# Optimization experiments

Hardware: AMD Instinct MI355X
Metric: run time of the kernel (lower is better)

## Reference

```python
import jax, jax.numpy as jnp
import numpy as np

CUTOFF = 10.0
NUM_GAUSSIANS = 50
LOG2 = float(np.log(2.0))
PI = float(np.pi)


def ssp(v):
    # shifted softplus: softplus(x) - log(2)
    return jax.nn.softplus(v) - LOG2


def setup_inputs() -> dict:
    key = jax.random.key(0)
    ks = jax.random.split(key, 16)
    N, E, H, F, G, L = 10000, 320000, 128, 128, NUM_GAUSSIANS, 6
    s = 0.08  # param scale to keep activations stable over 6 layers
    return {
        "x": jax.random.randint(ks[0], (N,), 0, 100),
        "edge_index": jax.random.randint(ks[1], (2, E), 0, N),
        "edge_dist": jax.random.uniform(ks[2], (E,), jnp.float32) * CUTOFF,
        "emb": jax.random.normal(ks[3], (100, H), jnp.float32) * s,
        "mlp_w1": jax.random.normal(ks[4], (L, G, F), jnp.float32) * s,
        "mlp_b1": jnp.zeros((L, F), jnp.float32),
        "mlp_w2": jax.random.normal(ks[5], (L, F, F), jnp.float32) * s,
        "mlp_b2": jnp.zeros((L, F), jnp.float32),
        "lin1_w": jax.random.normal(ks[6], (L, H, F), jnp.float32) * s,
        "lin2_w": jax.random.normal(ks[7], (L, F, H), jnp.float32) * s,
        "lin2_b": jnp.zeros((L, H), jnp.float32),
        "lin_w": jax.random.normal(ks[8], (L, H, H), jnp.float32) * s,
        "lin_b": jnp.zeros((L, H), jnp.float32),
        "out1_w": jax.random.normal(ks[9], (H, H // 2), jnp.float32) * s,
        "out1_b": jnp.zeros((H // 2,), jnp.float32),
        "out2_w": jax.random.normal(ks[10], (H // 2, H // 2), jnp.float32) * s,
        "out2_b": jnp.zeros((H // 2,), jnp.float32),
        "ro_w": jax.random.normal(ks[11], (H // 2, 12), jnp.float32) * s,
        "ro_b": jnp.zeros((12,), jnp.float32),
    }


def reference(x, edge_index, edge_dist, emb, mlp_w1, mlp_b1, mlp_w2, mlp_b2,
              lin1_w, lin2_w, lin2_b, lin_w, lin_b,
              out1_w, out1_b, out2_w, out2_b, ro_w, ro_b):
    N = x.shape[0]
    L = mlp_w1.shape[0]
    src, dst = edge_index[0], edge_index[1]

    h = emb[x]  # [N, H]

    # Gaussian smearing of distances -> [E, G]
    offset = jnp.linspace(0.0, CUTOFF, NUM_GAUSSIANS)
    coeff = -0.5 / (offset[1] - offset[0]) ** 2
    ea = jnp.exp(coeff * (edge_dist[:, None] - offset[None, :]) ** 2)

    # cosine cutoff envelope C [E]
    C = 0.5 * (jnp.cos(edge_dist * PI / CUTOFF) + 1.0)

    for l in range(L):
        # per-edge filter: MLP(gaussian) * cutoff  -> [E, F]
        W = (ssp(ea @ mlp_w1[l] + mlp_b1[l]) @ mlp_w2[l] + mlp_b2[l]) * C[:, None]
        xf = h @ lin1_w[l]                      # [N, F] (lin1, no bias)
        msg = xf[src] * W                       # gather + elementwise [E, F]
        agg = jax.ops.segment_sum(msg, dst, num_segments=N)  # scatter-add
        conv = agg @ lin2_w[l] + lin2_b[l]      # [N, H]
        h = h + (ssp(conv) @ lin_w[l] + lin_b[l])

    t = ssp(h @ out1_w + out1_b)
    t = t @ out2_w + out2_b
    h_agg = jnp.sum(t, axis=0)                  # [H//2]
    return h_agg @ ro_w + ro_b                  # [12]
```

## Files before the change

kernel.cpp:

```cpp
#include <hip/hip_runtime.h>
#include <math.h>

#define E_NUM 320000
#define N_NUM 10000
#define NB16  (N_NUM / 16)
#define TAB   2048

typedef unsigned short ushort_t;
typedef short short8_t __attribute__((ext_vector_type(8)));
typedef float f32x4    __attribute__((ext_vector_type(4)));

#define WP_O1   294912
#define WP_O2   303104
#define WP_W1T  307200
#define WP_W2T  356352
#define WP_TOT  454656

#define HB  1250
#define PB  ((WP_TOT + 255) / 256)

#define FK_SC 625
#define FK_TB 768
#define FK_EM NB16

__device__ __forceinline__ float ssp_f(float x) {
    return fmaxf(x, 0.f) + __logf(1.f + __expf(-fabsf(x))) - 0.69314718056f;
}

__device__ __forceinline__ float bf2f(ushort_t u) {
    union { unsigned int i; float f; } v;
    v.i = ((unsigned int)u) << 16;
    return v.f;
}
__device__ __forceinline__ ushort_t f2bf(float f) {
    union { float f; unsigned int i; } v;
    v.f = f;
    unsigned int u = v.i;
    unsigned int r = (u + 0x7FFFu + ((u >> 16) & 1u)) >> 16;
    return (ushort_t)r;
}

__global__ __launch_bounds__(256) void hist_pack_kernel(const int* __restrict__ ei,
                                                        int* __restrict__ counts,
                                                        const float* __restrict__ lin2_w,
                                                        const float* __restrict__ lin_w,
                                                        const float* __restrict__ lin1_w,
                                                        const float* __restrict__ o1w,
                                                        const float* __restrict__ o2w,
                                                        const float* __restrict__ mlp_w1,
                                                        const float* __restrict__ mlp_w2,
                                                        short* __restrict__ wpack) {
    if (blockIdx.x < HB) {
        int e = blockIdx.x * 256 + threadIdx.x;
        atomicAdd(&counts[ei[E_NUM + e]], 1);
        return;
    }
    int idx = (blockIdx.x - HB) * 256 + threadIdx.x;
    const int M128 = 16384;
    if (idx < 18 * M128) {
        int g = idx / M128, r = idx % M128;
        const float* src;
        if (g < 6) src = lin2_w + g * M128;
        else if (g < 12) src = lin_w + (g - 6) * M128;
        else src = lin1_w + (g - 12) * M128;
        int j = r & 7, L = (r >> 3) & 63, ks = (r >> 9) & 3, t = r >> 11;
        int n = t * 16 + (L & 15);
        int k = ks * 32 + (L >> 4) * 8 + j;
        wpack[idx] = (short)f2bf(src[k * 128 + n]);
    } else if (idx < WP_O2) {
        int r = idx - WP_O1;
        int j = r & 7, L = (r >> 3) & 63, ks = (r >> 9) & 3, t = r >> 11;
        int n = t * 16 + (L & 15);
        int k = ks * 32 + (L >> 4) * 8 + j;
        wpack[idx] = (short)f2bf(o1w[k * 64 + n]);
    } else if (idx < WP_W1T) {
        int r = idx - WP_O2;
        int j = r & 7, L = (r >> 3) & 63, ks = (r >> 9) & 1, t = r >> 10;
        int n = t * 16 + (L & 15);
        int k = ks * 32 + (L >> 4) * 8 + j;
        wpack[idx] = (short)f2bf(o2w[k * 64 + n]);
    } else if (idx < WP_W1T + 6 * 8192 && idx >= WP_W1T) {
        int r2 = idx - WP_W1T;
        int g = r2 / 8192, r = r2 % 8192;
        int j = r & 7, L = (r >> 3) & 63, ks = (r >> 9) & 1, t = r >> 10;
        int n = t * 16 + (L & 15);
        int k = ks * 32 + (L >> 4) * 8 + j;
        float v = (k < 50) ? mlp_w1[g * 6400 + k * 128 + n] : 0.f;
        wpack[idx] = (short)f2bf(v);
    } else if (idx < WP_TOT) {
        int r2 = idx - WP_W2T;
        int g = r2 / M128, r = r2 % M128;
        int j = r & 7, L = (r >> 3) & 63, ks = (r >> 9) & 3, t = r >> 11;
        int n = t * 16 + (L & 15);
        int k = ks * 32 + (L >> 4) * 8 + j;
        wpack[idx] = (short)f2bf(mlp_w2[g * M128 + k * 128 + n]);
    }
}

__global__ __launch_bounds__(1024) void scan_kernel(const int* __restrict__ counts,
                                                    int* __restrict__ offs,
                                                    int* __restrict__ cursor) {
    __shared__ int part[1024];
    const int tid = threadIdx.x;
    const int CH = 10;
    int base = tid * CH;
    int s = 0;
    #pragma unroll
    for (int i = 0; i < CH; ++i) {
        int idx = base + i;
        if (idx < N_NUM) s += counts[idx];
    }
    part[tid] = s;
    __syncthreads();
    for (int off = 1; off < 1024; off <<= 1) {
        int v = (tid >= off) ? part[tid - off] : 0;
        __syncthreads();
        part[tid] += v;
        __syncthreads();
    }
    int run = (tid > 0) ? part[tid - 1] : 0;
    #pragma unroll
    for (int i = 0; i < CH; ++i) {
        int idx = base + i;
        if (idx < N_NUM) {
            offs[idx] = run;
            cursor[idx] = run;
            run += counts[idx];
        }
    }
    if (tid == 1023) offs[N_NUM] = part[1023];
}

__global__ __launch_bounds__(512) void front_kernel(const int* __restrict__ ei,
                                                    const float* __restrict__ dist,
                                                    int* __restrict__ cursor,
                                                    int* __restrict__ meta,
                                                    const short* __restrict__ w1t,
                                                    const float* __restrict__ mlp_b1,
                                                    const short* __restrict__ w2t,
                                                    const float* __restrict__ mlp_b2,
                                                    ushort_t* __restrict__ tabB,
                                                    const int* __restrict__ x,
                                                    const float* __restrict__ emb,
                                                    const short* __restrict__ w1p0,
                                                    float* __restrict__ h,
                                                    ushort_t* __restrict__ xf) {
    __shared__ short EA[16 * 72];
    __shared__ short HD[16 * 136];
    __shared__ int s_x[16];
    const int tid = threadIdx.x;

    if (blockIdx.x < FK_SC) {
        int e = blockIdx.x * 512 + tid;
        int d = ei[E_NUM + e];
        int pos = atomicAdd(&cursor[d], 1);
        float t = dist[e] * ((float)(TAB - 1) / 10.0f);
        int i0 = (int)(t + 0.5f);
        if (i0 > TAB - 1) i0 = TAB - 1;
        meta[pos] = (i0 << 14) | ei[e];
        return;
    }

    const int wv = tid >> 6;
    const int lane = tid & 63;
    const int m = lane & 15, q = lane >> 4;

    if (blockIdx.x < FK_SC + FK_TB) {
        const int bt = blockIdx.x - FK_SC;
        const int l = bt >> 7;
        const int r0 = (bt & 127) * 16;
        const float DG = 10.0f / (float)(TAB - 1);
        const float STEP = 10.0f / 49.0f;
        const float COEFF = -0.5f / (STEP * STEP);

        for (int i = tid; i < 16 * 64; i += 512) {
            int r = i >> 6, k = i & 63;
            float v = 0.f;
            if (k < 50) {
                float d = (float)(r0 + r) * DG;
                float t = d - (float)k * STEP;
                v = __expf(COEFF * t * t);
            }
            EA[r * 72 + k] = (short)f2bf(v);
        }
        __syncthreads();

        {
            f32x4 acc = {0.f, 0.f, 0.f, 0.f};
            #pragma unroll
            for (int ks = 0; ks < 2; ++ks) {
                short8_t a = *(const short8_t*)(EA + m * 72 + ks * 32 + q * 8);
                short8_t b = *(const short8_t*)(w1t + l * 8192 + (wv * 2 + ks) * 512 + lane * 8);
                acc = __builtin_amdgcn_mfma_f32_16x16x32_bf16(a, b, acc, 0, 0, 0);
            }
            float bv = mlp_b1[l * 128 + wv * 16 + m];
            #pragma unroll
            for (int i = 0; i < 4; ++i)
                HD[(q * 4 + i) * 136 + wv * 16 + m] = (short)f2bf(ssp_f(acc[i] + bv));
        }
        __syncthreads();

        {
            f32x4 acc = {0.f, 0.f, 0.f, 0.f};
            #pragma unroll
            for (int ks = 0; ks < 4; ++ks) {
                short8_t a = *(const short8_t*)(HD + m * 136 + ks * 32 + q * 8);
                short8_t b = *(const short8_t*)(w2t + l * 16384 + (wv * 4 + ks) * 512 + lane * 8);
                acc = __builtin_amdgcn_mfma_f32_16x16x32_bf16(a, b, acc, 0, 0, 0);
            }
            int col = wv * 16 + m;
            float bv = mlp_b2[l * 128 + col];
            ushort_t* tl = tabB + (size_t)l * TAB * 128;
            #pragma unroll
            for (int i = 0; i < 4; ++i) {
                int row = r0 + q * 4 + i;
                float d = (float)row * DG;
                float C = 0.5f * (__cosf(d * 0.31415926535f) + 1.0f);
                tl[(size_t)row * 128 + col] = f2bf((acc[i] + bv) * C);
            }
        }
        return;
    }

    {
        const int n0 = (blockIdx.x - FK_SC - FK_TB) * 16;
        if (tid < 16) s_x[tid] = x[n0 + tid];
        __syncthreads();
        {
            int r = tid >> 5;
            int c4 = (tid & 31) * 4;
            float4 v = *(const float4*)(emb + (size_t)s_x[r] * 128 + c4);
            *(float4*)(h + (size_t)(n0 + r) * 128 + c4) = v;
            short4 o;
            o.x = (short)f2bf(v.x); o.y = (short)f2bf(v.y);
            o.z = (short)f2bf(v.z); o.w = (short)f2bf(v.w);
            *(short4*)(HD + r * 136 + c4) = o;
        }
        __syncthreads();
        f32x4 acc = {0.f, 0.f, 0.f, 0.f};
        #pragma unroll
        for (int ks = 0; ks < 4; ++ks) {
            short8_t a = *(const short8_t*)(HD + m * 136 + ks * 32 + q * 8);
            short8_t b = *(const short8_t*)(w1p0 + (wv * 4 + ks) * 512 + lane * 8);
            acc = __builtin_amdgcn_mfma_f32_16x16x32_bf16(a, b, acc, 0, 0, 0);
        }
        #pragma unroll
        for (int i = 0; i < 4; ++i) {
            int grow = n0 + q * 4 + i;
            xf[(size_t)grow * 128 + wv * 16 + m] = f2bf(acc[i]);
        }
    }
}

__device__ __forceinline__ void nacc8(short8_t x, short8_t t, float* o) {
    #pragma unroll
    for (int j = 0; j < 8; ++j)
        o[j] = fmaf(bf2f((ushort_t)x[j]), bf2f((ushort_t)t[j]), o[j]);
}

template <bool LAST>
__global__ __launch_bounds__(512) void layer_kernel(const int* __restrict__ offs,
                                                    const int* __restrict__ meta,
                                                    const ushort_t* __restrict__ xf,
                                                    const ushort_t* __restrict__ tabB,
                                                    const short* __restrict__ w2p,
                                                    const float* __restrict__ lin2_b,
                                                    const short* __restrict__ wlp,
                                                    const float* __restrict__ lin_b,
                                                    const short* __restrict__ w1p,
                                                    float* __restrict__ h,
                                                    ushort_t* __restrict__ xf_out,
                                                    const short* __restrict__ o1p,
                                                    const float* __restrict__ o1b,
                                                    const short* __restrict__ o2p,
                                                    const float* __restrict__ o2b,
                                                    float* __restrict__ gs) {
    __shared__ short A1[16 * 136];
    __shared__ short A2[16 * 136];
    __shared__ float P[16 * 128];
    __shared__ float red[4][64];
    const int tid = threadIdx.x;
    const int n0 = blockIdx.x * 16;
    const int wv = tid >> 6;
    const int lane = tid & 63;
    const int strm = wv >> 2;

    {
        const int qt = lane >> 4;
        const int c8 = (lane & 15) * 8;
        const int row = (wv & 3) * 4 + qt;
        const int node = n0 + row;
        int s0 = offs[node];
        int s1 = offs[node + 1];
        int mid = s0 + ((s1 - s0) >> 1);
        int e   = strm ? mid : s0;
        int end = strm ? s1  : mid;

        float accA[8] = {0.f, 0.f, 0.f, 0.f, 0.f, 0.f, 0.f, 0.f};
        float accB[8] = {0.f, 0.f, 0.f, 0.f, 0.f, 0.f, 0.f, 0.f};

        int mc[8];
        bool have = (e + 8 <= end);
        if (have) {
            #pragma unroll
            for (int u = 0; u < 8; ++u) mc[u] = meta[e + u];
        }
        while (have) {
            bool nxt = (e + 16 <= end);
            int mn[8];
            if (nxt) {
                #pragma unroll
                for (int u = 0; u < 8; ++u) mn[u] = meta[e + 8 + u];
            }
            short8_t xv[8], tv[8];
            #pragma unroll
            for (int u = 0; u < 8; ++u) {
                xv[u] = *(const short8_t*)(xf + (size_t)(mc[u] & 0x3FFF) * 128 + c8);
                tv[u] = *(const short8_t*)(tabB + (size_t)((unsigned)mc[u] >> 14) * 128 + c8);
            }
            #pragma unroll
            for (int u = 0; u < 8; ++u)
                nacc8(xv[u], tv[u], (u & 1) ? accB : accA);
            #pragma unroll
            for (int u = 0; u < 8; ++u) mc[u] = mn[u];
            e += 8;
            have = nxt;
        }
        if (e + 4 <= end) {
            int mm[4];
            #pragma unroll
            for (int u = 0; u < 4; ++u) mm[u] = meta[e + u];
            short8_t xv[4], tv[4];
            #pragma unroll
            for (int u = 0; u < 4; ++u) {
                xv[u] = *(const short8_t*)(xf + (size_t)(mm[u] & 0x3FFF) * 128 + c8);
                tv[u] = *(const short8_t*)(tabB + (size_t)((unsigned)mm[u] >> 14) * 128 + c8);
            }
            #pragma unroll
            for (int u = 0; u < 4; ++u)
                nacc8(xv[u], tv[u], (u & 1) ? accB : accA);
            e += 4;
        }
        for (; e < end; ++e) {
            int mm = meta[e];
            short8_t xv = *(const short8_t*)(xf + (size_t)(mm & 0x3FFF) * 128 + c8);
            short8_t tv = *(const short8_t*)(tabB + (size_t)((unsigned)mm >> 14) * 128 + c8);
            nacc8(xv, tv, accA);
        }

        if (!strm) {
            #pragma unroll
            for (int j = 0; j < 8; ++j)
                P[row * 128 + c8 + j] = accA[j] + accB[j];
        }
        __syncthreads();
        if (strm) {
            short8_t out;
            #pragma unroll
            for (int j = 0; j < 8; ++j)
                out[j] = (short)f2bf(accA[j] + accB[j] + P[row * 128 + c8 + j]);
            *(short8_t*)&A1[row * 136 + c8] = out;
        }
    }
    __syncthreads();

    const int m = lane & 15, q = lane >> 4;
    const int t = wv;

    {
        f32x4 acc = {0.f, 0.f, 0.f, 0.f};
        #pragma unroll
        for (int ks = 0; ks < 4; ++ks) {
            short8_t a = *(const short8_t*)(A1 + m * 136 + ks * 32 + q * 8);
            short8_t b = *(const short8_t*)(w2p + (t * 4 + ks) * 512 + lane * 8);
            acc = __builtin_amdgcn_mfma_f32_16x16x32_bf16(a, b, acc, 0, 0, 0);
        }
        float bv = lin2_b[t * 16 + m];
        #pragma unroll
        for (int i = 0; i < 4; ++i)
            A2[(q * 4 + i) * 136 + t * 16 + m] = (short)f2bf(ssp_f(acc[i] + bv));
    }
    __syncthreads();

    {
        f32x4 acc = {0.f, 0.f, 0.f, 0.f};
        #pragma unroll
        for (int ks = 0; ks < 4; ++ks) {
            short8_t a = *(const short8_t*)(A2 + m * 136 + ks * 32 + q * 8);
            short8_t b = *(const short8_t*)(wlp + (t * 4 + ks) * 512 + lane * 8);
            acc = __builtin_amdgcn_mfma_f32_16x16x32_bf16(a, b, acc, 0, 0, 0);
        }
        float bv = lin_b[t * 16 + m];
        #pragma unroll
        for (int i = 0; i < 4; ++i) {
            int r = q * 4 + i;
            int grow = n0 + r;
            float h0 = h[(size_t)grow * 128 + t * 16 + m];
            float hn = h0 + acc[i] + bv;
            if (!LAST) h[(size_t)grow * 128 + t * 16 + m] = hn;
            A1[r * 136 + t * 16 + m] = (short)f2bf(hn);
        }
    }
    __syncthreads();

    if constexpr (!LAST) {
        f32x4 acc = {0.f, 0.f, 0.f, 0.f};
        #pragma unroll
        for (int ks = 0; ks < 4; ++ks) {
            short8_t a = *(const short8_t*)(A1 + m * 136 + ks * 32 + q * 8);
            short8_t b = *(const short8_t*)(w1p + (t * 4 + ks) * 512 + lane * 8);
            acc = __builtin_amdgcn_mfma_f32_16x16x32_bf16(a, b, acc, 0, 0, 0);
        }
        #pragma unroll
        for (int i = 0; i < 4; ++i) {
            int r = q * 4 + i;
            int grow = n0 + r;
            xf_out[(size_t)grow * 128 + t * 16 + m] = f2bf(acc[i]);
        }
    } else {
        if (wv < 4) {
            f32x4 acc = {0.f, 0.f, 0.f, 0.f};
            #pragma unroll
            for (int ks = 0; ks < 4; ++ks) {
                short8_t a = *(const short8_t*)(A1 + m * 136 + ks * 32 + q * 8);
                short8_t b = *(const short8_t*)(o1p + (wv * 4 + ks) * 512 + lane * 8);
                acc = __builtin_amdgcn_mfma_f32_16x16x32_bf16(a, b, acc, 0, 0, 0);
            }
            float bv = o1b[wv * 16 + m];
            #pragma unroll
            for (int i = 0; i < 4; ++i) {
                int r = q * 4 + i;
                A2[r * 136 + wv * 16 + m] = (short)f2bf(ssp_f(acc[i] + bv));
            }
        }
        __syncthreads();
        if (wv < 4) {
            f32x4 acc = {0.f, 0.f, 0.f, 0.f};
            #pragma unroll
            for (int ks = 0; ks < 2; ++ks) {
                short8_t a = *(const short8_t*)(A2 + m * 136 + ks * 32 + q * 8);
                short8_t b = *(const short8_t*)(o2p + (wv * 2 + ks) * 512 + lane * 8);
                acc = __builtin_amdgcn_mfma_f32_16x16x32_bf16(a, b, acc, 0, 0, 0);
            }
            float bv = o2b[wv * 16 + m];
            float part = acc[0] + acc[1] + acc[2] + acc[3] + 4.0f * bv;
            red[q][wv * 16 + m] = part;
        }
        __syncthreads();
        if (tid < 64) {
            float s = red[0][tid] + red[1][tid] + red[2][tid] + red[3][tid];
            atomicAdd(&gs[tid], s);
        }
    }
}

__global__ void final_kernel(const float* __restrict__ gs,
                             const float* __restrict__ ro_w,
                             const float* __restrict__ ro_b,
                             float* __restrict__ out) {
    int i = threadIdx.x;
    if (i < 12) {
        float s = ro_b[i];
        for (int k = 0; k < 64; ++k) s = fmaf(gs[k], ro_w[k * 12 + i], s);
        out[i] = s;
    }
}

extern "C" void kernel_launch(void* const* d_in, const int* in_sizes, int n_in,
                              void* d_out, int out_size, void* d_ws, size_t ws_size,
                              hipStream_t stream) {
    const int*   x      = (const int*)d_in[0];
    const int*   ei     = (const int*)d_in[1];
    const float* dist   = (const float*)d_in[2];
    const float* emb    = (const float*)d_in[3];
    const float* mlp_w1 = (const float*)d_in[4];
    const float* mlp_b1 = (const float*)d_in[5];
    const float* mlp_w2 = (const float*)d_in[6];
    const float* mlp_b2 = (const float*)d_in[7];
    const float* lin1_w = (const float*)d_in[8];
    const float* lin2_w = (const float*)d_in[9];
    const float* lin2_b = (const float*)d_in[10];
    const float* lin_w  = (const float*)d_in[11];
    const float* lin_b  = (const float*)d_in[12];
    const float* out1_w = (const float*)d_in[13];
    const float* out1_b = (const float*)d_in[14];
    const float* out2_w = (const float*)d_in[15];
    const float* out2_b = (const float*)d_in[16];
    const float* ro_w   = (const float*)d_in[17];
    const float* ro_b   = (const float*)d_in[18];
    float* out = (float*)d_out;

    char* base = (char*)d_ws;
    float*    h     = (float*)base;     base += (size_t)N_NUM * 128 * 4;
    ushort_t* tabB  = (ushort_t*)base;  base += (size_t)6 * TAB * 128 * 2;
    ushort_t* xf0   = (ushort_t*)base;  base += (size_t)N_NUM * 128 * 2;
    ushort_t* xf1   = (ushort_t*)base;  base += (size_t)N_NUM * 128 * 2;
    int*      meta  = (int*)base;       base += (size_t)E_NUM * 4;
    short*    wpack = (short*)base;     base += (size_t)WP_TOT * 2;
    float*    gs    = (float*)base;     base += 64 * 4;
    int*      offs  = (int*)base;       base += (N_NUM + 1) * 4;
    int*      cursor= (int*)base;       base += N_NUM * 4;
    int*      counts= (int*)base;       base += N_NUM * 4;

    hipMemsetAsync(counts, 0, N_NUM * sizeof(int), stream);
    hipMemsetAsync(gs, 0, 64 * sizeof(float), stream);

    hist_pack_kernel<<<HB + PB, 256, 0, stream>>>(
        ei, counts, lin2_w, lin_w, lin1_w, out1_w, out2_w, mlp_w1, mlp_w2, wpack);

    scan_kernel<<<1, 1024, 0, stream>>>(counts, offs, cursor);

    front_kernel<<<FK_SC + FK_TB + FK_EM, 512, 0, stream>>>(
        ei, dist, cursor, meta,
        wpack + WP_W1T, mlp_b1, wpack + WP_W2T, mlp_b2, tabB,
        x, emb, wpack + 12 * 16384, h, xf0);

    const short* o1p = wpack + WP_O1;
    const short* o2p = wpack + WP_O2;

    for (int l = 0; l < 6; ++l) {
        ushort_t* xin  = (l & 1) ? xf1 : xf0;
        ushort_t* xout = (l & 1) ? xf0 : xf1;
        const ushort_t* tl = tabB + (size_t)l * TAB * 128;
        const short* w2p = wpack + l * 16384;
        const short* wlp = wpack + (6 + l) * 16384;
        if (l < 5) {
            const short* w1p = wpack + (12 + l + 1) * 16384;
            layer_kernel<false><<<NB16, 512, 0, stream>>>(
                offs, meta, xin, tl,
                w2p, lin2_b + l * 128, wlp, lin_b + l * 128, w1p,
                h, xout, nullptr, nullptr, nullptr, nullptr, nullptr);
        } else {
            layer_kernel<true><<<NB16, 512, 0, stream>>>(
                offs, meta, xin, tl,
                w2p, lin2_b + l * 128, wlp, lin_b + l * 128, nullptr,
                h, nullptr, o1p, out1_b, o2p, out2_b, gs);
        }
    }

    final_kernel<<<1, 64, 0, stream>>>(gs, ro_w, ro_b, out);
}
```

Baseline: 288.3 us.

## Software-pipeline edge gather loop with 4-wide double buffering and occupancy hint

Restructures the per-node edge aggregation loop into a 4-edge software pipeline. The gathers for the next batch are issued before accumulating the current batch, and edge metadata is prefetched two batches ahead. The scalar tail loop becomes a single predicated 4-wide block, and launch_bounds adds a minimum of 4 blocks per CU to cap register use. The aim is to hide gather latency while keeping registers low, at the risk of spills or less memory-level parallelism than the old 8-wide batches.

```diff
diff --git a/kernel.cpp b/kernel.cpp
--- a/kernel.cpp
+++ b/kernel.cpp
@@ -259,7 +259,7 @@
 }
 
 template <bool LAST>
-__global__ __launch_bounds__(512) void layer_kernel(const int* __restrict__ offs,
+__global__ __launch_bounds__(512, 4) void layer_kernel(const int* __restrict__ offs,
                                                     const int* __restrict__ meta,
                                                     const ushort_t* __restrict__ xf,
                                                     const ushort_t* __restrict__ tabB,
@@ -299,37 +299,52 @@
         float accA[8] = {0.f, 0.f, 0.f, 0.f, 0.f, 0.f, 0.f, 0.f};
         float accB[8] = {0.f, 0.f, 0.f, 0.f, 0.f, 0.f, 0.f, 0.f};
 
-        int mc[8];
-        bool have = (e + 8 <= end);
-        if (have) {
-            #pragma unroll
-            for (int u = 0; u < 8; ++u) mc[u] = meta[e + u];
-        }
-        while (have) {
-            bool nxt = (e + 16 <= end);
-            int mn[8];
-            if (nxt) {
+        const int nb = (end - e) >> 2;
+        if (nb > 0) {
+            int mnxt[4] = {0, 0, 0, 0};
+            short8_t xv[4], tv[4];
+            {
+                int mcur[4];
                 #pragma unroll
-                for (int u = 0; u < 8; ++u) mn[u] = meta[e + 8 + u];
-            }
-            short8_t xv[8], tv[8];
-            #pragma unroll
-            for (int u = 0; u < 8; ++u) {
-                xv[u] = *(const short8_t*)(xf + (size_t)(mc[u] & 0x3FFF) * 128 + c8);
-                tv[u] = *(const short8_t*)(tabB + (size_t)((unsigned)mc[u] >> 14) * 128 + c8);
-            }
-            #pragma unroll
-            for (int u = 0; u < 8; ++u)
+                for (int u = 0; u < 4; ++u) mcur[u] = meta[e + u];
+                if (nb > 1) {
+                    #pragma unroll
+                    for (int u = 0; u < 4; ++u) mnxt[u] = meta[e + 4 + u];
+                }
+                #pragma unroll
+                for (int u = 0; u < 4; ++u) {
+                    xv[u] = *(const short8_t*)(xf + (size_t)(mcur[u] & 0x3FFF) * 128 + c8);
+                    tv[u] = *(const short8_t*)(tabB + (size_t)((unsigned)mcur[u] >> 14) * 128 + c8);
+                }
+            }
+            for (int b = 0; b < nb - 1; ++b) {
+                short8_t xn[4], tn[4];
+                #pragma unroll
+                for (int u = 0; u < 4; ++u) {
+                    xn[u] = *(const short8_t*)(xf + (size_t)(mnxt[u] & 0x3FFF) * 128 + c8);
+                    tn[u] = *(const short8_t*)(tabB + (size_t)((unsigned)mnxt[u] >> 14) * 128 + c8);
+                }
+                int mn2[4] = {0, 0, 0, 0};
+                if (b + 2 < nb) {
+                    #pragma unroll
+                    for (int u = 0; u < 4; ++u) mn2[u] = meta[e + 4 * (b + 2) + u];
+                }
+                #pragma unroll
+                for (int u = 0; u < 4; ++u)
+                    nacc8(xv[u], tv[u], (u & 1) ? accB : accA);
+                #pragma unroll
+                for (int u = 0; u < 4; ++u) { xv[u] = xn[u]; tv[u] = tn[u]; mnxt[u] = mn2[u]; }
+            }
+            #pragma unroll
+            for (int u = 0; u < 4; ++u)
                 nacc8(xv[u], tv[u], (u & 1) ? accB : accA);
-            #pragma unroll
-            for (int u = 0; u < 8; ++u) mc[u] = mn[u];
-            e += 8;
-            have = nxt;
-        }
-        if (e + 4 <= end) {
+            e += nb * 4;
+        }
+        int rem = end - e;
+        if (rem > 0) {
             int mm[4];
             #pragma unroll
-            for (int u = 0; u < 4; ++u) mm[u] = meta[e + u];
+            for (int u = 0; u < 4; ++u) mm[u] = meta[e + ((u < rem) ? u : 0)];
             short8_t xv[4], tv[4];
             #pragma unroll
             for (int u = 0; u < 4; ++u) {
@@ -338,14 +353,7 @@
             }
             #pragma unroll
             for (int u = 0; u < 4; ++u)
-                nacc8(xv[u], tv[u], (u & 1) ? accB : accA);
-            e += 4;
-        }
-        for (; e < end; ++e) {
-            int mm = meta[e];
-            short8_t xv = *(const short8_t*)(xf + (size_t)(mm & 0x3FFF) * 128 + c8);
-            short8_t tv = *(const short8_t*)(tabB + (size_t)((unsigned)mm >> 14) * 128 + c8);
-            nacc8(xv, tv, accA);
+                if (u < rem) nacc8(xv[u], tv[u], (u & 1) ? accB : accA);
         }
 
         if (!strm) {
```

After: 289.6 us. About the same (+0.5%).

## Replace global-atomic CSR build with per-chunk LDS histograms and chunked scatter

Applied to the files above, without the earlier changes.

Edge counting and CSR scatter now use 16 chunks, each histogrammed in shared memory and written out as a per-chunk count row. The scan kernel then derives a base offset for every chunk. The scatter step places edges using shared-memory atomic cursors initialised from those per-chunk bases, replacing the global atomics on a per-node cursor. The two memsets are removed, with gs zeroed inside the scan kernel. The trade-off is that the count and scatter phases now run on only 16 blocks, and the single-block scan has to read and write 16 times more data.

```diff
diff --git a/kernel.cpp b/kernel.cpp
--- a/kernel.cpp
+++ b/kernel.cpp
@@ -5,6 +5,9 @@
 #define N_NUM 10000
 #define NB16  (N_NUM / 16)
 #define TAB   2048
+
+#define NCHUNK 16
+#define CHSZ   (E_NUM / NCHUNK)
 
 typedef unsigned short ushort_t;
 typedef short short8_t __attribute__((ext_vector_type(8)));
@@ -16,10 +19,9 @@
 #define WP_W2T  356352
 #define WP_TOT  454656
 
-#define HB  1250
-#define PB  ((WP_TOT + 255) / 256)
-
-#define FK_SC 625
+#define PB512 (WP_TOT / 512)
+
+#define FK_SC NCHUNK
 #define FK_TB 768
 #define FK_EM NB16
 
@@ -40,8 +42,8 @@
     return (ushort_t)r;
 }
 
-__global__ __launch_bounds__(256) void hist_pack_kernel(const int* __restrict__ ei,
-                                                        int* __restrict__ counts,
+__global__ __launch_bounds__(512) void hist_pack_kernel(const int* __restrict__ ei,
+                                                        int* __restrict__ counts2d,
                                                         const float* __restrict__ lin2_w,
                                                         const float* __restrict__ lin_w,
                                                         const float* __restrict__ lin1_w,
@@ -50,12 +52,21 @@
                                                         const float* __restrict__ mlp_w1,
                                                         const float* __restrict__ mlp_w2,
                                                         short* __restrict__ wpack) {
-    if (blockIdx.x < HB) {
-        int e = blockIdx.x * 256 + threadIdx.x;
-        atomicAdd(&counts[ei[E_NUM + e]], 1);
+    if (blockIdx.x < NCHUNK) {
+        __shared__ int hist[N_NUM];
+        const int tid = threadIdx.x;
+        for (int i = tid; i < N_NUM; i += 512) hist[i] = 0;
+        __syncthreads();
+        const int base = blockIdx.x * CHSZ;
+        for (int r = tid; r < CHSZ; r += 512) {
+            atomicAdd(&hist[ei[E_NUM + base + r]], 1);
+        }
+        __syncthreads();
+        int* row = counts2d + blockIdx.x * N_NUM;
+        for (int i = tid; i < N_NUM; i += 512) row[i] = hist[i];
         return;
     }
-    int idx = (blockIdx.x - HB) * 256 + threadIdx.x;
+    int idx = (blockIdx.x - NCHUNK) * 512 + threadIdx.x;
     const int M128 = 16384;
     if (idx < 18 * M128) {
         int g = idx / M128, r = idx % M128;
@@ -79,7 +90,7 @@
         int n = t * 16 + (L & 15);
         int k = ks * 32 + (L >> 4) * 8 + j;
         wpack[idx] = (short)f2bf(o2w[k * 64 + n]);
-    } else if (idx < WP_W1T + 6 * 8192 && idx >= WP_W1T) {
+    } else if (idx < WP_W2T) {
         int r2 = idx - WP_W1T;
         int g = r2 / 8192, r = r2 % 8192;
         int j = r & 7, L = (r >> 3) & 63, ks = (r >> 9) & 1, t = r >> 10;
@@ -97,19 +108,29 @@
     }
 }
 
-__global__ __launch_bounds__(1024) void scan_kernel(const int* __restrict__ counts,
+__global__ __launch_bounds__(1024) void scan_kernel(const int* __restrict__ counts2d,
                                                     int* __restrict__ offs,
-                                                    int* __restrict__ cursor) {
+                                                    int* __restrict__ base2d,
+                                                    float* __restrict__ gs) {
     __shared__ int part[1024];
     const int tid = threadIdx.x;
     const int CH = 10;
-    int base = tid * CH;
+    if (tid < 64) gs[tid] = 0.f;
+
+    int tot[CH];
+    #pragma unroll
+    for (int i = 0; i < CH; ++i) tot[i] = 0;
+    for (int c = 0; c < NCHUNK; ++c) {
+        const int* row = counts2d + c * N_NUM;
+        #pragma unroll
+        for (int i = 0; i < CH; ++i) {
+            int b = tid * CH + i;
+            if (b < N_NUM) tot[i] += row[b];
+        }
+    }
     int s = 0;
     #pragma unroll
-    for (int i = 0; i < CH; ++i) {
-        int idx = base + i;
-        if (idx < N_NUM) s += counts[idx];
-    }
+    for (int i = 0; i < CH; ++i) s += tot[i];
     part[tid] = s;
     __syncthreads();
     for (int off = 1; off < 1024; off <<= 1) {
@@ -119,21 +140,34 @@
         __syncthreads();
     }
     int run = (tid > 0) ? part[tid - 1] : 0;
+    int off_i[CH];
     #pragma unroll
     for (int i = 0; i < CH; ++i) {
-        int idx = base + i;
-        if (idx < N_NUM) {
-            offs[idx] = run;
-            cursor[idx] = run;
-            run += counts[idx];
+        int b = tid * CH + i;
+        if (b < N_NUM) {
+            offs[b] = run;
+            off_i[i] = run;
+            run += tot[i];
         }
     }
     if (tid == 1023) offs[N_NUM] = part[1023];
+    for (int c = 0; c < NCHUNK; ++c) {
+        const int* row = counts2d + c * N_NUM;
+        int* brow = base2d + c * N_NUM;
+        #pragma unroll
+        for (int i = 0; i < CH; ++i) {
+            int b = tid * CH + i;
+            if (b < N_NUM) {
+                brow[b] = off_i[i];
+                off_i[i] += row[b];
+            }
+        }
+    }
 }
 
 __global__ __launch_bounds__(512) void front_kernel(const int* __restrict__ ei,
                                                     const float* __restrict__ dist,
-                                                    int* __restrict__ cursor,
+                                                    const int* __restrict__ base2d,
                                                     int* __restrict__ meta,
                                                     const short* __restrict__ w1t,
                                                     const float* __restrict__ mlp_b1,
@@ -145,25 +179,34 @@
                                                     const short* __restrict__ w1p0,
                                                     float* __restrict__ h,
                                                     ushort_t* __restrict__ xf) {
-    __shared__ short EA[16 * 72];
-    __shared__ short HD[16 * 136];
-    __shared__ int s_x[16];
+    __shared__ __align__(16) char smem[40960];
     const int tid = threadIdx.x;
 
     if (blockIdx.x < FK_SC) {
-        int e = blockIdx.x * 512 + tid;
-        int d = ei[E_NUM + e];
-        int pos = atomicAdd(&cursor[d], 1);
-        float t = dist[e] * ((float)(TAB - 1) / 10.0f);
-        int i0 = (int)(t + 0.5f);
-        if (i0 > TAB - 1) i0 = TAB - 1;
-        meta[pos] = (i0 << 14) | ei[e];
+        int* cur = (int*)smem;
+        const int c = blockIdx.x;
+        const int* brow = base2d + c * N_NUM;
+        for (int i = tid; i < N_NUM; i += 512) cur[i] = brow[i];
+        __syncthreads();
+        const int base = c * CHSZ;
+        for (int r = tid; r < CHSZ; r += 512) {
+            int e = base + r;
+            int d = ei[E_NUM + e];
+            int pos = atomicAdd(&cur[d], 1);
+            float t = dist[e] * ((float)(TAB - 1) / 10.0f);
+            int i0 = (int)(t + 0.5f);
+            if (i0 > TAB - 1) i0 = TAB - 1;
+            meta[pos] = (i0 << 14) | ei[e];
+        }
         return;
     }
 
     const int wv = tid >> 6;
     const int lane = tid & 63;
     const int m = lane & 15, q = lane >> 4;
+    short* EA = (short*)smem;
+    short* HD = (short*)(smem + 2304);
+    int*   s_x = (int*)(smem + 2304 + 4352);
 
     if (blockIdx.x < FK_SC + FK_TB) {
         const int bt = blockIdx.x - FK_SC;
@@ -499,19 +542,16 @@
     short*    wpack = (short*)base;     base += (size_t)WP_TOT * 2;
     float*    gs    = (float*)base;     base += 64 * 4;
     int*      offs  = (int*)base;       base += (N_NUM + 1) * 4;
-    int*      cursor= (int*)base;       base += N_NUM * 4;
-    int*      counts= (int*)base;       base += N_NUM * 4;
-
-    hipMemsetAsync(counts, 0, N_NUM * sizeof(int), stream);
-    hipMemsetAsync(gs, 0, 64 * sizeof(float), stream);
-
-    hist_pack_kernel<<<HB + PB, 256, 0, stream>>>(
-        ei, counts, lin2_w, lin_w, lin1_w, out1_w, out2_w, mlp_w1, mlp_w2, wpack);
-
-    scan_kernel<<<1, 1024, 0, stream>>>(counts, offs, cursor);
+    int*      counts2d = (int*)base;    base += (size_t)NCHUNK * N_NUM * 4;
+    int*      base2d   = (int*)base;    base += (size_t)NCHUNK * N_NUM * 4;
+
+    hist_pack_kernel<<<NCHUNK + PB512, 512, 0, stream>>>(
+        ei, counts2d, lin2_w, lin_w, lin1_w, out1_w, out2_w, mlp_w1, mlp_w2, wpack);
+
+    scan_kernel<<<1, 1024, 0, stream>>>(counts2d, offs, base2d, gs);
 
     front_kernel<<<FK_SC + FK_TB + FK_EM, 512, 0, stream>>>(
-        ei, dist, cursor, meta,
+        ei, dist, base2d, meta,
         wpack + WP_W1T, mlp_b1, wpack + WP_W2T, mlp_b2, tabB,
         x, emb, wpack + 12 * 16384, h, xf0);
 
```

Result: slower. 387.3 us (+34.4%).
